# Performance work log

Measured on AMD Instinct MI355X. Metric: run time of the kernel, lower is better.

Reference implementation:

```python
import jax, jax.numpy as jnp
import numpy as np

N_NODES = 100000
N_EDGES = 640000
D = 128


def setup_inputs() -> dict:
    key = jax.random.key(0)
    k1, k2, k3 = jax.random.split(key, 3)
    h = jax.random.normal(k1, (N_NODES, D), dtype=jnp.float32)
    edges = jax.random.randint(k2, (2, N_EDGES), 0, N_NODES, dtype=jnp.int64)
    W = jax.random.normal(k3, (1, D), dtype=jnp.float32) / np.sqrt(D)
    b = jnp.zeros((1,), dtype=jnp.float32)
    return {"h": h, "edges": edges, "W": W, "b": b}


def reference(h, edges, W, b):
    # gather source/object node features: [E, D]
    s = h[edges[0]]
    o = h[edges[1]]
    # tiny linear on fused elementwise sin(s - o): [E, 1]
    score = jnp.sin(s - o) @ W.T + b
    # pairwise softmax over consecutive edge pairs (torch F.softmax dim=1 on [E/2, 2])
    score = jax.nn.softmax(score.reshape(-1, 2), axis=1).reshape(-1, 1)
    return (score, score > 0.5)
```

## Files before the change

kernel.cpp:

```cpp
#include <hip/hip_runtime.h>


__global__ __launch_bounds__(256) void sine_predictor_kernel(
    const float* __restrict__ h,
    const int*   __restrict__ edges,
    const float* __restrict__ W,
    const float* __restrict__ b,
    float*       __restrict__ out,
    int n_edges)
{
    const int lane = threadIdx.x & 63;
    const int sub  = lane & 31;
    const int half = lane >> 5;
    const int waves_per_block = blockDim.x >> 6;
    const int wave_in_block   = threadIdx.x >> 6;
    const int n_pairs = n_edges >> 1;

    const float4 w4  = reinterpret_cast<const float4*>(W)[sub];
    const float bias = b[0];

    int pair = blockIdx.x * waves_per_block + wave_in_block;
    const int stride = gridDim.x * waves_per_block;

    for (; pair < n_pairs; pair += stride) {
        const int e   = 2 * pair + half;
        const int src = edges[e];
        const int obj = edges[n_edges + e];

        const float4 s4 = reinterpret_cast<const float4*>(h + (size_t)src * 128)[sub];
        const float4 o4 = reinterpret_cast<const float4*>(h + (size_t)obj * 128)[sub];

        float part = sinf(s4.x - o4.x) * w4.x
                   + sinf(s4.y - o4.y) * w4.y
                   + sinf(s4.z - o4.z) * w4.z
                   + sinf(s4.w - o4.w) * w4.w;

        #pragma unroll
        for (int m = 16; m >= 1; m >>= 1)
            part += __shfl_xor(part, m, 64);

        const float x     = part + bias;
        const float other = __shfl_xor(x, 32, 64);
        const float mx    = fmaxf(x, other);
        const float es    = __expf(x - mx);
        const float eo    = __expf(other - mx);
        const float p     = es / (es + eo);

        if (sub == 0) {
            out[e]           = p;
            out[n_edges + e] = (p > 0.5f) ? 1.0f : 0.0f;
        }
    }
}

extern "C" void kernel_launch(void* const* d_in, const int* in_sizes, int n_in,
                              void* d_out, int out_size, void* d_ws, size_t ws_size,
                              hipStream_t stream) {
    const float* h     = (const float*)d_in[0];
    const int*   edges = (const int*)d_in[1];
    const float* W     = (const float*)d_in[2];
    const float* b     = (const float*)d_in[3];
    float*       out   = (float*)d_out;

    const int n_edges = in_sizes[1] / 2;

    const int blocks = 2048;
    sine_predictor_kernel<<<blocks, 256, 0, stream>>>(h, edges, W, b, out, n_edges);
}
```

Baseline: 98.98 us.

## Gather bf16 copy of node features with fp32 fixup for near-tie pairs

Each call first casts h to a bf16 copy in workspace. The main kernel gathers the half-width rows, computes scores with fast intrinsics, and unrolls four pairs per wave iteration. Pairs whose logit gap falls below a small tolerance are appended to a list through an atomic counter. A third kernel recomputes those pairs in fp32 so the thresholded output stays consistent. This is meant to halve random-gather traffic, at the cost of an extra full pass over h, two more launches, and bf16 error in the stored probabilities.

```diff
diff --git a/kernel.cpp b/kernel.cpp
--- a/kernel.cpp
+++ b/kernel.cpp
@@ -1,7 +1,163 @@
 #include <hip/hip_runtime.h>
 
 
-__global__ __launch_bounds__(256) void sine_predictor_kernel(
+constexpr int   DIMS = 128;
+constexpr float TAU  = 0.05f;
+
+__device__ __forceinline__ float bf2f(unsigned short u) {
+    union { unsigned int i; float f; } c;
+    c.i = ((unsigned int)u) << 16;
+    return c.f;
+}
+
+__device__ __forceinline__ unsigned short f2bf_rne(float f) {
+    union { float f; unsigned int i; } c;
+    c.f = f;
+    unsigned int r = c.i + 0x7FFFu + ((c.i >> 16) & 1u);
+    return (unsigned short)(r >> 16);
+}
+
+__global__ __launch_bounds__(256) void cast_h_kernel(
+    const float* __restrict__ h, unsigned short* __restrict__ hb,
+    int n_vec4, int* __restrict__ counter)
+{
+    if (blockIdx.x == 0 && threadIdx.x == 0) *counter = 0;
+    int i = blockIdx.x * blockDim.x + threadIdx.x;
+    const int stride = gridDim.x * blockDim.x;
+    for (; i < n_vec4; i += stride) {
+        const float4 v = reinterpret_cast<const float4*>(h)[i];
+        ushort4 o;
+        o.x = f2bf_rne(v.x); o.y = f2bf_rne(v.y);
+        o.z = f2bf_rne(v.z); o.w = f2bf_rne(v.w);
+        reinterpret_cast<ushort4*>(hb)[i] = o;
+    }
+}
+
+__global__ __launch_bounds__(256) void score_bf16_kernel(
+    const unsigned short* __restrict__ hb,
+    const int*   __restrict__ edges,
+    const float* __restrict__ W,
+    const float* __restrict__ b,
+    float*       __restrict__ out,
+    int n_edges,
+    int* __restrict__ counter, int* __restrict__ list, int list_cap)
+{
+    const int lane = threadIdx.x & 63;
+    const int sub  = lane & 31;
+    const int half = lane >> 5;
+    const int waves_per_block = blockDim.x >> 6;
+    const int wave_id = blockIdx.x * waves_per_block + (threadIdx.x >> 6);
+    const int n_waves = gridDim.x * waves_per_block;
+    const int n_pairs = n_edges >> 1;
+    const int n_chunk = (n_pairs + 3) >> 2;
+
+    const float4 w4  = reinterpret_cast<const float4*>(W)[sub];
+    const float bias = b[0];
+
+    for (int c = wave_id; c < n_chunk; c += n_waves) {
+        const int base_pair = c * 4;
+        float x[4];
+        bool  valid[4];
+
+        #pragma unroll
+        for (int u = 0; u < 4; ++u) {
+            const int pair = base_pair + u;
+            valid[u] = pair < n_pairs;
+            x[u] = 0.0f;
+            if (valid[u]) {
+                const int e   = 2 * pair + half;
+                const int src = edges[e];
+                const int obj = edges[n_edges + e];
+                const ushort4 sv = reinterpret_cast<const ushort4*>(
+                                       hb + (size_t)src * DIMS)[sub];
+                const ushort4 ov = reinterpret_cast<const ushort4*>(
+                                       hb + (size_t)obj * DIMS)[sub];
+                x[u] = __sinf(bf2f(sv.x) - bf2f(ov.x)) * w4.x
+                     + __sinf(bf2f(sv.y) - bf2f(ov.y)) * w4.y
+                     + __sinf(bf2f(sv.z) - bf2f(ov.z)) * w4.z
+                     + __sinf(bf2f(sv.w) - bf2f(ov.w)) * w4.w;
+            }
+        }
+
+        #pragma unroll
+        for (int u = 0; u < 4; ++u) {
+            #pragma unroll
+            for (int m = 16; m >= 1; m >>= 1)
+                x[u] += __shfl_xor(x[u], m, 64);
+            x[u] += bias;
+        }
+
+        #pragma unroll
+        for (int u = 0; u < 4; ++u) {
+            if (!valid[u]) continue;
+            const int e      = 2 * (base_pair + u) + half;
+            const float other = __shfl_xor(x[u], 32, 64);
+            const float mx   = fmaxf(x[u], other);
+            const float es   = __expf(x[u] - mx);
+            const float eo   = __expf(other - mx);
+            const float p    = es / (es + eo);
+            if (sub == 0) {
+                out[e]           = p;
+                out[n_edges + e] = (p > 0.5f) ? 1.0f : 0.0f;
+            }
+            if (lane == 0 && fabsf(x[u] - other) < TAU) {
+                const int id = atomicAdd(counter, 1);
+                if (id < list_cap) list[id] = base_pair + u;
+            }
+        }
+    }
+}
+
+__global__ __launch_bounds__(256) void fixup_kernel(
+    const float* __restrict__ h,
+    const int*   __restrict__ edges,
+    const float* __restrict__ W,
+    const float* __restrict__ b,
+    float*       __restrict__ out,
+    int n_edges,
+    const int* __restrict__ counter, const int* __restrict__ list, int list_cap)
+{
+    const int lane = threadIdx.x & 63;
+    const int sub  = lane & 31;
+    const int half = lane >> 5;
+    const int waves_per_block = blockDim.x >> 6;
+    const int wave_id = blockIdx.x * waves_per_block + (threadIdx.x >> 6);
+    const int n_waves = gridDim.x * waves_per_block;
+
+    int cnt = *counter;
+    if (cnt > list_cap) cnt = list_cap;
+
+    const float4 w4  = reinterpret_cast<const float4*>(W)[sub];
+    const float bias = b[0];
+
+    for (int i = wave_id; i < cnt; i += n_waves) {
+        const int pair = list[i];
+        const int e    = 2 * pair + half;
+        const int src  = edges[e];
+        const int obj  = edges[n_edges + e];
+        const float4 s4 = reinterpret_cast<const float4*>(h + (size_t)src * DIMS)[sub];
+        const float4 o4 = reinterpret_cast<const float4*>(h + (size_t)obj * DIMS)[sub];
+        float part = __sinf(s4.x - o4.x) * w4.x
+                   + __sinf(s4.y - o4.y) * w4.y
+                   + __sinf(s4.z - o4.z) * w4.z
+                   + __sinf(s4.w - o4.w) * w4.w;
+        #pragma unroll
+        for (int m = 16; m >= 1; m >>= 1)
+            part += __shfl_xor(part, m, 64);
+        const float x     = part + bias;
+        const float other = __shfl_xor(x, 32, 64);
+        const float mx    = fmaxf(x, other);
+        const float es    = __expf(x - mx);
+        const float eo    = __expf(other - mx);
+        const float p     = es / (es + eo);
+        if (sub == 0) {
+            out[e]           = p;
+            out[n_edges + e] = (p > 0.5f) ? 1.0f : 0.0f;
+        }
+    }
+}
+
+__global__ __launch_bounds__(256) void sine_predictor_fp32_kernel(
     const float* __restrict__ h,
     const int*   __restrict__ edges,
     const float* __restrict__ W,
@@ -13,39 +169,32 @@
     const int sub  = lane & 31;
     const int half = lane >> 5;
     const int waves_per_block = blockDim.x >> 6;
-    const int wave_in_block   = threadIdx.x >> 6;
+    const int wave_id = blockIdx.x * waves_per_block + (threadIdx.x >> 6);
+    const int n_waves = gridDim.x * waves_per_block;
     const int n_pairs = n_edges >> 1;
 
     const float4 w4  = reinterpret_cast<const float4*>(W)[sub];
     const float bias = b[0];
 
-    int pair = blockIdx.x * waves_per_block + wave_in_block;
-    const int stride = gridDim.x * waves_per_block;
-
-    for (; pair < n_pairs; pair += stride) {
+    for (int pair = wave_id; pair < n_pairs; pair += n_waves) {
         const int e   = 2 * pair + half;
         const int src = edges[e];
         const int obj = edges[n_edges + e];
-
-        const float4 s4 = reinterpret_cast<const float4*>(h + (size_t)src * 128)[sub];
-        const float4 o4 = reinterpret_cast<const float4*>(h + (size_t)obj * 128)[sub];
-
-        float part = sinf(s4.x - o4.x) * w4.x
-                   + sinf(s4.y - o4.y) * w4.y
-                   + sinf(s4.z - o4.z) * w4.z
-                   + sinf(s4.w - o4.w) * w4.w;
-
+        const float4 s4 = reinterpret_cast<const float4*>(h + (size_t)src * DIMS)[sub];
+        const float4 o4 = reinterpret_cast<const float4*>(h + (size_t)obj * DIMS)[sub];
+        float part = __sinf(s4.x - o4.x) * w4.x
+                   + __sinf(s4.y - o4.y) * w4.y
+                   + __sinf(s4.z - o4.z) * w4.z
+                   + __sinf(s4.w - o4.w) * w4.w;
         #pragma unroll
         for (int m = 16; m >= 1; m >>= 1)
             part += __shfl_xor(part, m, 64);
-
         const float x     = part + bias;
         const float other = __shfl_xor(x, 32, 64);
         const float mx    = fmaxf(x, other);
         const float es    = __expf(x - mx);
         const float eo    = __expf(other - mx);
         const float p     = es / (es + eo);
-
         if (sub == 0) {
             out[e]           = p;
             out[n_edges + e] = (p > 0.5f) ? 1.0f : 0.0f;
@@ -63,7 +212,24 @@
     float*       out   = (float*)d_out;
 
     const int n_edges = in_sizes[1] / 2;
-
-    const int blocks = 2048;
-    sine_predictor_kernel<<<blocks, 256, 0, stream>>>(h, edges, W, b, out, n_edges);
-}
+    const int n_nodes = in_sizes[0] / DIMS;
+
+    const size_t hb_bytes = (size_t)n_nodes * DIMS * 2;
+    const size_t need     = hb_bytes + 16 + (1u << 20);
+
+    if (ws_size >= need) {
+        unsigned short* hb = (unsigned short*)d_ws;
+        int* counter = (int*)((char*)d_ws + hb_bytes);
+        int* list    = (int*)((char*)d_ws + hb_bytes + 16);
+        int list_cap = (int)((ws_size - hb_bytes - 16) / 4);
+        if (list_cap > n_edges / 2) list_cap = n_edges / 2;
+
+        cast_h_kernel<<<2048, 256, 0, stream>>>(h, hb, n_nodes * DIMS / 4, counter);
+        score_bf16_kernel<<<2048, 256, 0, stream>>>(hb, edges, W, b, out, n_edges,
+                                                    counter, list, list_cap);
+        fixup_kernel<<<512, 256, 0, stream>>>(h, edges, W, b, out, n_edges,
+                                              counter, list, list_cap);
+    } else {
+        sine_predictor_fp32_kernel<<<2048, 256, 0, stream>>>(h, edges, W, b, out, n_edges);
+    }
+}
```

After: 187.2 us. 89.1% more time.

## Process four edges per wave with 16 lanes each and two chunks in flight

Applied to the files above, without the earlier changes.

Each wave now handles four edges at a time, with 16 lanes per edge reading two float4s each, and processes two chunks per loop iteration so more gathers are outstanding at once. Precise sinf is replaced with the fast __sinf intrinsic. Launch bounds now request an occupancy hint and the grid shrinks to 1536 blocks. The aim is more memory-level parallelism on the random row gathers and cheaper transcendental math, at the cost of more registers and reduced sine accuracy.

```diff
diff --git a/kernel.cpp b/kernel.cpp
--- a/kernel.cpp
+++ b/kernel.cpp
@@ -1,7 +1,9 @@
 #include <hip/hip_runtime.h>
 
 
-__global__ __launch_bounds__(256) void sine_predictor_kernel(
+constexpr int DIMS = 128;
+
+__global__ __launch_bounds__(256, 6) void sine_predictor_kernel(
     const float* __restrict__ h,
     const int*   __restrict__ edges,
     const float* __restrict__ W,
@@ -9,46 +11,90 @@
     float*       __restrict__ out,
     int n_edges)
 {
-    const int lane = threadIdx.x & 63;
-    const int sub  = lane & 31;
-    const int half = lane >> 5;
-    const int waves_per_block = blockDim.x >> 6;
-    const int wave_in_block   = threadIdx.x >> 6;
-    const int n_pairs = n_edges >> 1;
+    const int lane    = threadIdx.x & 63;
+    const int sub     = lane & 15;
+    const int quarter = lane >> 4;
+    const int wave_id = blockIdx.x * (blockDim.x >> 6) + (threadIdx.x >> 6);
+    const int n_waves = gridDim.x * (blockDim.x >> 6);
+    const int n_ch    = (n_edges + 3) >> 2;
 
-    const float4 w4  = reinterpret_cast<const float4*>(W)[sub];
+    const float4 wl  = reinterpret_cast<const float4*>(W)[sub * 2 + 0];
+    const float4 wh  = reinterpret_cast<const float4*>(W)[sub * 2 + 1];
     const float bias = b[0];
 
-    int pair = blockIdx.x * waves_per_block + wave_in_block;
-    const int stride = gridDim.x * waves_per_block;
+    for (int c = wave_id; c < n_ch; c += 2 * n_waves) {
+        const int  c2   = c + n_waves;
+        const bool has2 = c2 < n_ch;
 
-    for (; pair < n_pairs; pair += stride) {
-        const int e   = 2 * pair + half;
-        const int src = edges[e];
-        const int obj = edges[n_edges + e];
+        const int eA  = 4 * c + quarter;
+        const int eAc = min(eA, n_edges - 1);
+        const int eB  = has2 ? 4 * c2 + quarter : eAc;
+        const int eBc = min(eB, n_edges - 1);
 
-        const float4 s4 = reinterpret_cast<const float4*>(h + (size_t)src * 128)[sub];
-        const float4 o4 = reinterpret_cast<const float4*>(h + (size_t)obj * 128)[sub];
+        const int srcA = edges[eAc];
+        const int objA = edges[n_edges + eAc];
+        const int srcB = edges[eBc];
+        const int objB = edges[n_edges + eBc];
 
-        float part = sinf(s4.x - o4.x) * w4.x
-                   + sinf(s4.y - o4.y) * w4.y
-                   + sinf(s4.z - o4.z) * w4.z
-                   + sinf(s4.w - o4.w) * w4.w;
+        const float4* sAr = reinterpret_cast<const float4*>(h + (size_t)srcA * DIMS);
+        const float4* oAr = reinterpret_cast<const float4*>(h + (size_t)objA * DIMS);
+        const float4* sBr = reinterpret_cast<const float4*>(h + (size_t)srcB * DIMS);
+        const float4* oBr = reinterpret_cast<const float4*>(h + (size_t)objB * DIMS);
+
+        const float4 sA0 = sAr[sub * 2 + 0];
+        const float4 sA1 = sAr[sub * 2 + 1];
+        const float4 oA0 = oAr[sub * 2 + 0];
+        const float4 oA1 = oAr[sub * 2 + 1];
+        const float4 sB0 = sBr[sub * 2 + 0];
+        const float4 sB1 = sBr[sub * 2 + 1];
+        const float4 oB0 = oBr[sub * 2 + 0];
+        const float4 oB1 = oBr[sub * 2 + 1];
+
+        float xA = __sinf(sA0.x - oA0.x) * wl.x
+                 + __sinf(sA0.y - oA0.y) * wl.y
+                 + __sinf(sA0.z - oA0.z) * wl.z
+                 + __sinf(sA0.w - oA0.w) * wl.w
+                 + __sinf(sA1.x - oA1.x) * wh.x
+                 + __sinf(sA1.y - oA1.y) * wh.y
+                 + __sinf(sA1.z - oA1.z) * wh.z
+                 + __sinf(sA1.w - oA1.w) * wh.w;
+        float xB = __sinf(sB0.x - oB0.x) * wl.x
+                 + __sinf(sB0.y - oB0.y) * wl.y
+                 + __sinf(sB0.z - oB0.z) * wl.z
+                 + __sinf(sB0.w - oB0.w) * wl.w
+                 + __sinf(sB1.x - oB1.x) * wh.x
+                 + __sinf(sB1.y - oB1.y) * wh.y
+                 + __sinf(sB1.z - oB1.z) * wh.z
+                 + __sinf(sB1.w - oB1.w) * wh.w;
 
         #pragma unroll
-        for (int m = 16; m >= 1; m >>= 1)
-            part += __shfl_xor(part, m, 64);
+        for (int m = 8; m >= 1; m >>= 1) xA += __shfl_xor(xA, m, 64);
+        #pragma unroll
+        for (int m = 8; m >= 1; m >>= 1) xB += __shfl_xor(xB, m, 64);
+        xA += bias;
+        xB += bias;
 
-        const float x     = part + bias;
-        const float other = __shfl_xor(x, 32, 64);
-        const float mx    = fmaxf(x, other);
-        const float es    = __expf(x - mx);
-        const float eo    = __expf(other - mx);
-        const float p     = es / (es + eo);
-
-        if (sub == 0) {
-            out[e]           = p;
-            out[n_edges + e] = (p > 0.5f) ? 1.0f : 0.0f;
+        {
+            const float other = __shfl_xor(xA, 16, 64);
+            const float mx = fmaxf(xA, other);
+            const float es = __expf(xA - mx);
+            const float eo = __expf(other - mx);
+            const float p  = es / (es + eo);
+            if (sub == 0 && eA < n_edges) {
+                out[eA]           = p;
+                out[n_edges + eA] = (p > 0.5f) ? 1.0f : 0.0f;
+            }
+        }
+        if (has2) {
+            const float other = __shfl_xor(xB, 16, 64);
+            const float mx = fmaxf(xB, other);
+            const float es = __expf(xB - mx);
+            const float eo = __expf(other - mx);
+            const float p  = es / (es + eo);
+            if (sub == 0 && eB < n_edges) {
+                out[eB]           = p;
+                out[n_edges + eB] = (p > 0.5f) ? 1.0f : 0.0f;
+            }
         }
     }
 }
@@ -64,6 +110,6 @@
 
     const int n_edges = in_sizes[1] / 2;
 
-    const int blocks = 2048;
+    const int blocks = 1536;
     sine_predictor_kernel<<<blocks, 256, 0, stream>>>(h, edges, W, b, out, n_edges);
 }
```

New measurement: 90.94 us. 8.1% less time.

## Process four edges per wave with software-pipelined gathers and fast sine

Applied to the files above, without the earlier changes.

Each wave now handles four edges (16 lanes per edge, two float4 per lane) instead of two, and the loop is software-pipelined with double-buffered index and row loads so gathers for later chunks are in flight while the current chunk computes. sinf is replaced with __sinf, and the softmax is simplified to a sigmoid form. The intent is to hide gather latency and reduce ALU cost; __sinf loses accuracy for large arguments and the unrolled pipeline raises register use.

```diff
diff --git a/kernel.cpp b/kernel.cpp
--- a/kernel.cpp
+++ b/kernel.cpp
@@ -1,5 +1,7 @@
 #include <hip/hip_runtime.h>
 
+
+constexpr int DIMS = 128;
 
 __global__ __launch_bounds__(256) void sine_predictor_kernel(
     const float* __restrict__ h,
@@ -9,48 +11,87 @@
     float*       __restrict__ out,
     int n_edges)
 {
-    const int lane = threadIdx.x & 63;
-    const int sub  = lane & 31;
-    const int half = lane >> 5;
-    const int waves_per_block = blockDim.x >> 6;
-    const int wave_in_block   = threadIdx.x >> 6;
-    const int n_pairs = n_edges >> 1;
+    const int lane    = threadIdx.x & 63;
+    const int sub     = lane & 15;
+    const int quarter = lane >> 4;
+    const int wave_id = blockIdx.x * (blockDim.x >> 6) + (threadIdx.x >> 6);
+    const int n       = gridDim.x * (blockDim.x >> 6);
+    const int n_ch    = (n_edges + 3) >> 2;
 
-    const float4 w4  = reinterpret_cast<const float4*>(W)[sub];
+    const float4 wl  = reinterpret_cast<const float4*>(W)[sub * 2 + 0];
+    const float4 wh  = reinterpret_cast<const float4*>(W)[sub * 2 + 1];
     const float bias = b[0];
 
-    int pair = blockIdx.x * waves_per_block + wave_in_block;
-    const int stride = gridDim.x * waves_per_block;
+    #define LOAD_IDX(ch, iS, iO)                                   \
+        {                                                          \
+            const int e_  = 4 * (ch) + quarter;                    \
+            const int ec_ = min(e_, n_edges - 1);                  \
+            iS = edges[ec_];                                       \
+            iO = edges[n_edges + ec_];                             \
+        }
 
-    for (; pair < n_pairs; pair += stride) {
-        const int e   = 2 * pair + half;
-        const int src = edges[e];
-        const int obj = edges[n_edges + e];
+    #define LOAD_ROWS(iS, iO, s0, s1, o0, o1)                                  \
+        {                                                                      \
+            const float4* sr_ = reinterpret_cast<const float4*>(h + (size_t)(iS) * DIMS); \
+            const float4* or_ = reinterpret_cast<const float4*>(h + (size_t)(iO) * DIMS); \
+            s0 = sr_[sub * 2 + 0];                                             \
+            s1 = sr_[sub * 2 + 1];                                             \
+            o0 = or_[sub * 2 + 0];                                             \
+            o1 = or_[sub * 2 + 1];                                             \
+        }
 
-        const float4 s4 = reinterpret_cast<const float4*>(h + (size_t)src * 128)[sub];
-        const float4 o4 = reinterpret_cast<const float4*>(h + (size_t)obj * 128)[sub];
+    #define COMPUTE_STORE(ch, s0, s1, o0, o1)                                  \
+        {                                                                      \
+            float x_ = __sinf(s0.x - o0.x) * wl.x + __sinf(s0.y - o0.y) * wl.y \
+                     + __sinf(s0.z - o0.z) * wl.z + __sinf(s0.w - o0.w) * wl.w \
+                     + __sinf(s1.x - o1.x) * wh.x + __sinf(s1.y - o1.y) * wh.y \
+                     + __sinf(s1.z - o1.z) * wh.z + __sinf(s1.w - o1.w) * wh.w;\
+            _Pragma("unroll")                                                  \
+            for (int m_ = 8; m_ >= 1; m_ >>= 1) x_ += __shfl_xor(x_, m_, 64);  \
+            x_ += bias;                                                        \
+            const float other_ = __shfl_xor(x_, 16, 64);                       \
+            const float p_ = 1.0f / (1.0f + __expf(other_ - x_));              \
+            const int e_ = 4 * (ch) + quarter;                                 \
+            if (sub == 0 && e_ < n_edges) {                                    \
+                out[e_]           = p_;                                        \
+                out[n_edges + e_] = (p_ > 0.5f) ? 1.0f : 0.0f;                 \
+            }                                                                  \
+        }
 
-        float part = sinf(s4.x - o4.x) * w4.x
-                   + sinf(s4.y - o4.y) * w4.y
-                   + sinf(s4.z - o4.z) * w4.z
-                   + sinf(s4.w - o4.w) * w4.w;
+    int c = wave_id;
+    if (c >= n_ch) return;
 
-        #pragma unroll
-        for (int m = 16; m >= 1; m >>= 1)
-            part += __shfl_xor(part, m, 64);
+    int iS_a, iO_a;
+    LOAD_IDX(min(c, n_ch - 1), iS_a, iO_a);
+    float4 a_s0, a_s1, a_o0, a_o1;
+    LOAD_ROWS(iS_a, iO_a, a_s0, a_s1, a_o0, a_o1);
+    int iS_b, iO_b;
+    LOAD_IDX(min(c + n, n_ch - 1), iS_b, iO_b);
 
-        const float x     = part + bias;
-        const float other = __shfl_xor(x, 32, 64);
-        const float mx    = fmaxf(x, other);
-        const float es    = __expf(x - mx);
-        const float eo    = __expf(other - mx);
-        const float p     = es / (es + eo);
+    while (c < n_ch) {
+        float4 b_s0, b_s1, b_o0, b_o1;
+        LOAD_ROWS(iS_b, iO_b, b_s0, b_s1, b_o0, b_o1);
+        int iS_a2, iO_a2;
+        LOAD_IDX(min(c + 2 * n, n_ch - 1), iS_a2, iO_a2);
+        __builtin_amdgcn_sched_barrier(0);
+        COMPUTE_STORE(c, a_s0, a_s1, a_o0, a_o1);
 
-        if (sub == 0) {
-            out[e]           = p;
-            out[n_edges + e] = (p > 0.5f) ? 1.0f : 0.0f;
+        LOAD_ROWS(iS_a2, iO_a2, a_s0, a_s1, a_o0, a_o1);
+        int iS_b2, iO_b2;
+        LOAD_IDX(min(c + 3 * n, n_ch - 1), iS_b2, iO_b2);
+        __builtin_amdgcn_sched_barrier(0);
+        if (c + n < n_ch) {
+            COMPUTE_STORE(c + n, b_s0, b_s1, b_o0, b_o1);
         }
+
+        iS_b = iS_b2;
+        iO_b = iO_b2;
+        c += 2 * n;
     }
+
+    #undef LOAD_IDX
+    #undef LOAD_ROWS
+    #undef COMPUTE_STORE
 }
 
 extern "C" void kernel_launch(void* const* d_in, const int* in_sizes, int n_in,
```

Result: faster. 91.28 us (-7.8%).
